# Kernel tuning notes

Measured on AMD Instinct MI355X. Metric: run time of the kernel, lower is better.

## Reference

```python
import jax, jax.numpy as jnp
import numpy as np

B, T, D, H = 4, 2048, 1024, 16
DK, DV, K, I = 48, 96, 4, 3072
EPS = 1e-5


def rmsnorm(x, w, eps=EPS):
    return x * jax.lax.rsqrt(jnp.mean(x * x, -1, keepdims=True) + eps) * w


def l2norm(x, eps=1e-6):
    return x * jax.lax.rsqrt(jnp.sum(x * x, -1, keepdims=True) + eps)


def causal_conv(x, w):
    # x: [B,T,C], w: [C,K]; causal depthwise conv (torch cross-correlation semantics)
    k = w.shape[1]
    xp = jnp.pad(x, ((0, 0), (k - 1, 0), (0, 0))).transpose(0, 2, 1)  # [B,C,T+K-1]
    y = jax.lax.conv_general_dilated(xp, w[:, None, :], (1,), 'VALID',
                                     feature_group_count=w.shape[0])
    return y.transpose(0, 2, 1)


def gated_delta_rule(q, k, v, g, beta):
    # q,k: [B,T,H,DK]  v: [B,T,H,DV]  g,beta: [B,T,H]
    scale = q.shape[-1] ** -0.5
    qT = jnp.moveaxis(q, 1, 0) * scale
    kT = jnp.moveaxis(k, 1, 0)
    vT = jnp.moveaxis(v, 1, 0)
    gT = jnp.moveaxis(g, 1, 0)
    bT = jnp.moveaxis(beta, 1, 0)
    S0 = jnp.zeros((q.shape[0], q.shape[2], q.shape[3], v.shape[3]), q.dtype)

    def step(S, inp):
        q_t, k_t, v_t, g_t, b_t = inp
        S = S * jnp.exp(g_t)[..., None, None]                      # gated decay
        v_new = (v_t - jnp.einsum('bhk,bhkv->bhv', k_t, S)) * b_t[..., None]
        S = S + k_t[..., None] * v_new[..., None, :]               # delta-rule update
        o_t = jnp.einsum('bhk,bhkv->bhv', q_t, S)
        return S, o_t

    _, o = jax.lax.scan(step, S0, (qT, kT, vT, gT, bT))
    return jnp.moveaxis(o, 0, 1)


def setup_inputs() -> dict:
    key = jax.random.key(0)
    ks = jax.random.split(key, 20)
    s = 0.02
    return {
        'hidden_states': jax.random.normal(ks[0], (B, T, D), jnp.float32),
        'norm1_w': jnp.ones((D,), jnp.float32),
        'q_w': jax.random.normal(ks[1], (D, H * DK), jnp.float32) * s,
        'k_w': jax.random.normal(ks[2], (D, H * DK), jnp.float32) * s,
        'v_w': jax.random.normal(ks[3], (D, H * DV), jnp.float32) * s,
        'conv_q_w': jax.random.normal(ks[4], (H * DK, K), jnp.float32) * 0.2,
        'conv_k_w': jax.random.normal(ks[5], (H * DK, K), jnp.float32) * 0.2,
        'conv_v_w': jax.random.normal(ks[6], (H * DV, K), jnp.float32) * 0.2,
        'b_w': jax.random.normal(ks[7], (D, H), jnp.float32) * s,
        'a_w': jax.random.normal(ks[8], (D, H), jnp.float32) * s,
        'A_log': jnp.log(jax.random.uniform(ks[9], (H,), jnp.float32, 1.0, 16.0)),
        'dt_bias': jax.random.normal(ks[10], (H,), jnp.float32) * 0.5,
        'g_w': jax.random.normal(ks[11], (D, H * DV), jnp.float32) * s,
        'o_norm_w': jnp.ones((DV,), jnp.float32),
        'o_w': jax.random.normal(ks[12], (H * DV, D), jnp.float32) * s,
        'norm2_w': jnp.ones((D,), jnp.float32),
        'gate_w': jax.random.normal(ks[13], (D, I), jnp.float32) * s,
        'up_w': jax.random.normal(ks[14], (D, I), jnp.float32) * s,
        'down_w': jax.random.normal(ks[15], (I, D), jnp.float32) * s,
    }


def reference(hidden_states, norm1_w, q_w, k_w, v_w, conv_q_w, conv_k_w, conv_v_w,
              b_w, a_w, A_log, dt_bias, g_w, o_norm_w, o_w, norm2_w,
              gate_w, up_w, down_w):
    x = hidden_states
    h = rmsnorm(x, norm1_w)
    # --- GatedDeltaNet mixer ---
    q = jax.nn.silu(causal_conv(h @ q_w, conv_q_w)).reshape(B, T, H, DK)
    k = jax.nn.silu(causal_conv(h @ k_w, conv_k_w)).reshape(B, T, H, DK)
    v = jax.nn.silu(causal_conv(h @ v_w, conv_v_w)).reshape(B, T, H, DV)
    q, k = l2norm(q), l2norm(k)
    beta = jax.nn.sigmoid(h @ b_w)                                  # [B,T,H]
    g = -jnp.exp(A_log) * jax.nn.softplus(h @ a_w + dt_bias)        # [B,T,H] mamba gate
    o = gated_delta_rule(q, k, v, g, beta)                          # [B,T,H,DV]
    gate = (h @ g_w).reshape(B, T, H, DV)
    o = rmsnorm(o, o_norm_w) * (gate * jax.nn.sigmoid(gate))        # fused gated RMSNorm
    x = x + o.reshape(B, T, H * DV) @ o_w
    # --- SwiGLU MLP ---
    h2 = rmsnorm(x, norm2_w)
    x = x + (jax.nn.silu(h2 @ gate_w) * (h2 @ up_w)) @ down_w
    return x
```

## Files before the change

kernel.cpp:

```cpp
#include <hip/hip_runtime.h>
#include <hip/hip_bf16.h>
#include <math.h>

constexpr int Bn = 4, Tn = 2048, Dn = 1024, Hn = 16, DKn = 48, DVn = 96, In = 3072;
constexpr int BT = Bn * Tn;
constexpr int HDK = Hn * DKn;
constexpr int HDV = Hn * DVn;
constexpr int QKVC = 2 * HDK + HDV;
constexpr int CC = 64;
constexpr int NC = Tn / CC;

using bf16 = __hip_bfloat16;
typedef __attribute__((ext_vector_type(8))) short bf16x8;
typedef __attribute__((ext_vector_type(4))) float f32x4;

constexpr size_t WO_HBF   = 0;
constexpr size_t WO_QKVR  = 16777216;
constexpr size_t WO_OSC   = 16777216;
constexpr size_t WO_ACT   = 16777216;
constexpr size_t WO_A     = 16777216;
constexpr size_t WO_B     = 26214400;
constexpr size_t WO_ST    = 45088768;
constexpr size_t WO_QKVC  = 67108864;
constexpr size_t WO_GATE  = 117440512;
constexpr size_t WO_X1    = 142606336;
constexpr size_t WO_BA    = 176160768;
constexpr size_t WO_GC    = 177209344;
constexpr size_t WO_T     = 177733632;
constexpr size_t WO_UV    = 194510848;
constexpr size_t WO_WB    = 219676672;
constexpr size_t WB_QKVT = 0;
constexpr size_t WB_GT   = 3145728;
constexpr size_t WB_OT   = 4718592;
constexpr size_t WB_GATET= 6291456;
constexpr size_t WB_UPT  = 9437184;
constexpr size_t WB_DOWNT= 12582912;
constexpr size_t WB_ABT  = 15728640;

__device__ __forceinline__ float sigmoidf_(float x) { return 1.f / (1.f + __expf(-x)); }
__device__ __forceinline__ float siluf(float x) { return x * sigmoidf_(x); }

__device__ __forceinline__ void glds16(const void* g, void* l) {
  __builtin_amdgcn_global_load_lds((const __attribute__((address_space(1))) void*)g,
                                   (__attribute__((address_space(3))) void*)l, 16, 0, 0);
}

__device__ __forceinline__ f32x4 mfma16(bf16x8 a, bf16x8 b, f32x4 c) {
  return __builtin_amdgcn_mfma_f32_16x16x32_bf16(a, b, c, 0, 0, 0);
}

__device__ __forceinline__ bf16x8 scale8(bf16x8 a, float s) {
  bf16x8 r;
#pragma unroll
  for (int e = 0; e < 8; e++) {
    float f = __bfloat162float(__ushort_as_bfloat16((unsigned short)a[e])) * s;
    r[e] = (short)__bfloat16_as_ushort(__float2bfloat16(f));
  }
  return r;
}

__device__ __forceinline__ float b2f(short u) {
  return __bfloat162float(__ushort_as_bfloat16((unsigned short)u));
}
__device__ __forceinline__ short f2b(float f) {
  return (short)__bfloat16_as_ushort(__float2bfloat16(f));
}

struct TcastArgs {
  const float* src[10];
  bf16* dst[10];
  int R[10], C[10], gxw[10], t0[10];
};

__global__ void tcast_all(TcastArgs a) {
  __shared__ float t[32][33];
  int bid = blockIdx.x;
  int i = 0;
#pragma unroll
  for (int k = 1; k < 10; k++) if (bid >= a.t0[k]) i = k;
  int lt = bid - a.t0[i];
  int gxw = a.gxw[i];
  int bx = lt % gxw, by = lt / gxw;
  const float* in = a.src[i];
  bf16* out = a.dst[i];
  int R = a.R[i], C = a.C[i];
  int tx = threadIdx.x, ty = threadIdx.y;
  int c0 = bx * 32, r0 = by * 32;
#pragma unroll
  for (int j = 0; j < 4; j++) {
    int r = ty + j * 8;
    float v = (c0 + tx < C) ? in[(size_t)(r0 + r) * C + c0 + tx] : 0.f;
    t[r][tx] = v;
  }
  __syncthreads();
#pragma unroll
  for (int j = 0; j < 4; j++) {
    int cc = ty + j * 8;
    if (c0 + cc < C) out[(size_t)(c0 + cc) * R + r0 + tx] = __float2bfloat16(t[tx][cc]);
  }
}

__global__ void rmsnorm_bf_k(const float* __restrict__ x, const float* __restrict__ w,
                             bf16* __restrict__ y) {
  int row = blockIdx.x;
  const float4* xr = (const float4*)(x + (size_t)row * Dn);
  int tid = threadIdx.x;
  float4 v = xr[tid];
  float ss = v.x * v.x + v.y * v.y + v.z * v.z + v.w * v.w;
  for (int m = 32; m >= 1; m >>= 1) ss += __shfl_xor(ss, m, 64);
  __shared__ float wsum[4];
  if ((tid & 63) == 0) wsum[tid >> 6] = ss;
  __syncthreads();
  ss = wsum[0] + wsum[1] + wsum[2] + wsum[3];
  float rs = rsqrtf(ss * (1.f / Dn) + 1e-5f);
  float4 wv = ((const float4*)w)[tid];
  bf16* yr = y + (size_t)row * Dn + tid * 4;
  yr[0] = __float2bfloat16(v.x * rs * wv.x);
  yr[1] = __float2bfloat16(v.y * rs * wv.y);
  yr[2] = __float2bfloat16(v.z * rs * wv.z);
  yr[3] = __float2bfloat16(v.w * rs * wv.w);
}

#define AS256(bi) (lds + (bi) * 8192)
#define BS256(bi) (lds + 32768 + (bi) * 8192)
#define STAGE256(bi, k0) do { \
    glds16(gA0 + (k0), AS256(bi) + w * 512); \
    glds16(gA1 + (k0), AS256(bi) + 4096 + w * 512); \
    glds16(gB0 + (k0), BS256(bi) + w * 512); \
    glds16(gB1 + (k0), BS256(bi) + 4096 + w * 512); \
  } while (0)

__global__ __launch_bounds__(512, 2) void gemm256(
    const bf16* __restrict__ A, const bf16* __restrict__ Bt,
    bf16* __restrict__ C0, bf16* __restrict__ C1,
    int gx, int N, int K, int mode) {
  __shared__ bf16 lds[65536];
  int nb = gx * 32;
  int q8 = nb >> 3;
  int bid = blockIdx.x;
  int sw = (bid & 7) * q8 + (bid >> 3);
  int by = sw & 31, bx = sw >> 5;
  int bm = by * 256, bn = bx * 256;
  int tid = threadIdx.x;
  int lane = tid & 63, w = tid >> 6;
  int l15 = lane & 15, lq = lane >> 4;
  int wr = w >> 2, wc = w & 3;
  int arow0 = tid >> 2;
  int srcq = (tid & 3) ^ ((arow0 >> 1) & 3);
  const bf16* gA0 = A + (size_t)(bm + arow0) * K + srcq * 8;
  const bf16* gA1 = A + (size_t)(bm + 128 + arow0) * K + srcq * 8;
  const bf16* gB0 = Bt + (size_t)(bn + arow0) * K + srcq * 8;
  const bf16* gB1 = Bt + (size_t)(bn + 128 + arow0) * K + srcq * 8;
  int slot = lq ^ ((l15 >> 1) & 3);
  f32x4 acc[8][4];
#pragma unroll
  for (int m = 0; m < 8; m++)
#pragma unroll
    for (int n = 0; n < 4; n++) acc[m][n] = (f32x4){0.f, 0.f, 0.f, 0.f};
  int NT = K >> 5;
  STAGE256(0, 0);
  STAGE256(1, 32);
  STAGE256(2, 64);
  for (int t = 0; t < NT; ++t) {
    int b = t & 3;
    if (t <= NT - 3)      { asm volatile("s_waitcnt vmcnt(8)" ::: "memory"); }
    else if (t == NT - 2) { asm volatile("s_waitcnt vmcnt(4)" ::: "memory"); }
    else                  { asm volatile("s_waitcnt vmcnt(0)" ::: "memory"); }
    __builtin_amdgcn_s_barrier();
    bf16x8 af[8], bfr[4];
#pragma unroll
    for (int m = 0; m < 8; m++)
      af[m] = *(const bf16x8*)(AS256(b) + (wr * 128 + m * 16 + l15) * 32 + slot * 8);
#pragma unroll
    for (int n = 0; n < 4; n++)
      bfr[n] = *(const bf16x8*)(BS256(b) + (wc * 64 + n * 16 + l15) * 32 + slot * 8);
    __builtin_amdgcn_s_setprio(1);
#pragma unroll
    for (int m = 0; m < 8; m++)
#pragma unroll
      for (int n = 0; n < 4; n++)
        acc[m][n] = mfma16(af[m], bfr[n], acc[m][n]);
    __builtin_amdgcn_s_setprio(0);
    if (t + 3 < NT) STAGE256((t + 3) & 3, (t + 3) * 32);
  }
  __syncthreads();
  bf16* dst; int ldc, bnl; bool doSilu;
  if (mode == 10) {
    if (bn < 3072) { dst = C0; ldc = 3072; bnl = bn; doSilu = false; }
    else           { dst = C1; ldc = 1536; bnl = bn - 3072; doSilu = false; }
  } else {
    if (bn < 3072) { dst = C0; ldc = 3072; bnl = bn; doSilu = true; }
    else           { dst = C1; ldc = 3072; bnl = bn - 3072; doSilu = false; }
  }
  bf16* cw = lds + w * 8192;
#pragma unroll
  for (int m = 0; m < 8; m++)
#pragma unroll
    for (int n = 0; n < 4; n++)
#pragma unroll
      for (int i = 0; i < 4; i++) {
        int row_l = m * 16 + lq * 4 + i;
        int col_l = n * 16 + l15;
        float v = acc[m][n][i];
        if (doSilu) v = siluf(v);
        cw[row_l * 64 + col_l] = __float2bfloat16(v);
      }
  __syncthreads();
  int r8 = lane >> 3, c8 = (lane & 7) * 8;
#pragma unroll
  for (int it = 0; it < 16; it++) {
    int row_l = it * 8 + r8;
    bf16x8 val = *(const bf16x8*)&cw[row_l * 64 + c8];
    *(bf16x8*)&dst[(size_t)(bm + wr * 128 + row_l) * ldc + bnl + wc * 64 + c8] = val;
  }
}

#define STAGE128(bi, k0) do { \
    { int c0_ = 2 * w4; \
      int arow_ = bm + c0_ * 16 + srow; \
      glds16(A + (size_t)arow_ * K + (k0) + gq * 8, &As[bi][c0_ * 512]); \
      int brow_ = bn + c0_ * 16 + srow; if (brow_ >= N) brow_ = 0; \
      glds16(Bt + (size_t)brow_ * K + (k0) + gq * 8, &Bs[bi][c0_ * 512]); \
      int c1_ = c0_ + 1; \
      int arow2_ = bm + c1_ * 16 + srow; \
      glds16(A + (size_t)arow2_ * K + (k0) + gq * 8, &As[bi][c1_ * 512]); \
      int brow2_ = bn + c1_ * 16 + srow; if (brow2_ >= N) brow2_ = 0; \
      glds16(Bt + (size_t)brow2_ * K + (k0) + gq * 8, &Bs[bi][c1_ * 512]); \
    } \
  } while (0)

__global__ __launch_bounds__(256) void gemm_mfma(
    const bf16* __restrict__ A, const bf16* __restrict__ Bt,
    void* __restrict__ Cv, const float* __restrict__ res,
    int N, int K, int ldc, int mode) {
  __shared__ bf16 As[4][4096];
  __shared__ bf16 Bs[4][4096];
  int tid = threadIdx.x, lane = tid & 63, w4 = tid >> 6;
  int bm = blockIdx.y * 128, bn = blockIdx.x * 128;
  int wr = w4 >> 1, wc = w4 & 1;
  int srow = lane >> 2;
  int gq = (lane & 3) ^ ((lane >> 3) & 3);
  int qa = (lane >> 4) ^ ((lane >> 1) & 3);
  int arow_base = wr * 64 + (lane & 15);
  int brow_base = wc * 64 + (lane & 15);
  f32x4 acc[4][4];
#pragma unroll
  for (int m = 0; m < 4; m++)
#pragma unroll
    for (int n = 0; n < 4; n++) acc[m][n] = (f32x4){0.f, 0.f, 0.f, 0.f};
  int NT = K >> 5;
  STAGE128(0, 0);
  STAGE128(1, 32);
  STAGE128(2, 64);
  for (int t = 0; t < NT; ++t) {
    int b = t & 3;
    if (t <= NT - 3)      { asm volatile("s_waitcnt vmcnt(8)" ::: "memory"); }
    else if (t == NT - 2) { asm volatile("s_waitcnt vmcnt(4)" ::: "memory"); }
    else                  { asm volatile("s_waitcnt vmcnt(0)" ::: "memory"); }
    __builtin_amdgcn_s_barrier();
    bf16x8 af[4], bfr[4];
#pragma unroll
    for (int m = 0; m < 4; m++)
      af[m] = *(const bf16x8*)&As[b][(arow_base + m * 16) * 32 + qa * 8];
#pragma unroll
    for (int n = 0; n < 4; n++)
      bfr[n] = *(const bf16x8*)&Bs[b][(brow_base + n * 16) * 32 + qa * 8];
    __builtin_amdgcn_s_setprio(1);
#pragma unroll
    for (int m = 0; m < 4; m++)
#pragma unroll
      for (int n = 0; n < 4; n++)
        acc[m][n] = mfma16(af[m], bfr[n], acc[m][n]);
    __builtin_amdgcn_s_setprio(0);
    if (t + 3 < NT) STAGE128((t + 3) & 3, (t + 3) * 32);
  }
#pragma unroll
  for (int m = 0; m < 4; m++) {
#pragma unroll
    for (int n = 0; n < 4; n++) {
      int col = bn + wc * 64 + n * 16 + (lane & 15);
      if (col >= N) continue;
#pragma unroll
      for (int i = 0; i < 4; i++) {
        int row = bm + wr * 64 + m * 16 + (lane >> 4) * 4 + i;
        float v = acc[m][n][i];
        size_t idx = (size_t)row * ldc + col;
        if (mode == 0) {
          if (res) v += res[idx];
          ((float*)Cv)[idx] = v;
        } else {
          ((bf16*)Cv)[idx] = __float2bfloat16(v);
        }
      }
    }
  }
}

__global__ __launch_bounds__(256) void convsilu2_k(const bf16* __restrict__ in,
                                                   bf16* __restrict__ outp,
                                                   const float* __restrict__ wq,
                                                   const float* __restrict__ wk,
                                                   const float* __restrict__ wv) {
  int tx = threadIdx.x & 31;
  int ty = threadIdx.x >> 5;
  int c = (blockIdx.x * 32 + tx) * 8;
  int gt = blockIdx.y * 8 + ty;
  int b = gt >> 11, t = gt & (Tn - 1);
  const float* wsrc = (c < HDK) ? (wq + c * 4)
                     : (c < 2 * HDK) ? (wk + (c - HDK) * 4)
                                     : (wv + (c - 2 * HDK) * 4);
  float4 W[8];
#pragma unroll
  for (int j = 0; j < 8; j++) W[j] = ((const float4*)wsrc)[j];
  const bf16* base = in + (size_t)b * Tn * QKVC + c;
  bf16x8 r[4];
  bf16x8 zero = {0, 0, 0, 0, 0, 0, 0, 0};
#pragma unroll
  for (int j = 0; j < 4; j++) {
    int tt = t - 3 + j;
    r[j] = (tt >= 0) ? *(const bf16x8*)(base + (size_t)tt * QKVC) : zero;
  }
  bf16x8 o;
#pragma unroll
  for (int ch = 0; ch < 8; ch++) {
    float x0 = b2f(r[0][ch]), x1 = b2f(r[1][ch]), x2 = b2f(r[2][ch]), x3 = b2f(r[3][ch]);
    float y = x0 * W[ch].x + x1 * W[ch].y + x2 * W[ch].z + x3 * W[ch].w;
    o[ch] = f2b(siluf(y));
  }
  *(bf16x8*)(outp + (size_t)gt * QKVC + c) = o;
}

__global__ __launch_bounds__(256) void l2norm_k(bf16* __restrict__ qkv) {
  int row = blockIdx.x * 256 + threadIdx.x;
  int t = row >> 5, hr = row & 31;
  bf16* p = qkv + (size_t)t * QKVC + hr * DKn;
  bf16x8 v[6];
  float ss = 0.f;
#pragma unroll
  for (int j = 0; j < 6; j++) {
    v[j] = *(const bf16x8*)(p + j * 8);
#pragma unroll
    for (int e = 0; e < 8; e++) { float f = b2f(v[j][e]); ss += f * f; }
  }
  float rs = rsqrtf(ss + 1e-6f);
#pragma unroll
  for (int j = 0; j < 6; j++) {
    bf16x8 o;
#pragma unroll
    for (int e = 0; e < 8; e++) o[e] = f2b(b2f(v[j][e]) * rs);
    *(bf16x8*)(p + j * 8) = o;
  }
}

__global__ void betag_k(float* __restrict__ ba, const float* __restrict__ A_log,
                        const float* __restrict__ dt_bias) {
  int i = blockIdx.x * blockDim.x + threadIdx.x;
  int h = i & 15, r = i >> 4;
  float bv = ba[(size_t)r * 32 + h];
  float av = ba[(size_t)r * 32 + 16 + h];
  ba[(size_t)r * 32 + h] = sigmoidf_(bv);
  float xx = av + dt_bias[h];
  float sp = (xx > 20.f) ? xx : log1pf(__expf(xx));
  ba[(size_t)r * 32 + 16 + h] = -__expf(A_log[h]) * sp;
}

__global__ __launch_bounds__(256) void dn_p1a(const bf16* __restrict__ qkv,
                                              const float* __restrict__ ba,
                                              float* __restrict__ Gc_g,
                                              bf16* __restrict__ T_g,
                                              bf16* __restrict__ Uv_g,
                                              bf16* __restrict__ A_g,
                                              bf16* __restrict__ B_g) {
  __shared__ __align__(16) char smem[62976];
  bf16 (*Kl)[72]   = (bf16(*)[72])(smem);
  bf16 (*Tl)[72]   = (bf16(*)[72])(smem + 9216);
  bf16 (*UvdT)[72] = (bf16(*)[72])(smem + 18432);
  float* Gcl = (float*)(smem + 32256);
  float* Bl  = (float*)(smem + 32512);
  bf16 (*Vl)[100]  = (bf16(*)[100])(smem + 32768);
  float (*Nl)[68]  = (float(*)[68])(smem + 45568);
  bf16 (*KTl)[72]  = (bf16(*)[72])(smem + 32768);
  bf16 (*KTbl)[72] = (bf16(*)[72])(smem + 39680);
  bf16 (*M2T)[72]  = (bf16(*)[72])(smem + 46592);
  int cid = blockIdx.x;
  int nc = cid & (NC - 1);
  int bh = cid >> 5;
  int h = bh & 15, b = bh >> 4;
  int t0 = nc * CC;
  int tid = threadIdx.x, lane = tid & 63, w = tid >> 6;
  int l15 = lane & 15, qd = lane >> 4;
  bf16 zb = __float2bfloat16(0.f);
  {
    int t = tid >> 2, p = tid & 3;
    const bf16* row = qkv + ((size_t)(b * Tn + t0 + t)) * QKVC;
    int c0 = p * 12;
#pragma unroll
    for (int j = 0; j < 12; ++j) Kl[t][c0 + j] = row[HDK + h * DKn + c0 + j];
    int j0 = p * 24;
#pragma unroll
    for (int j = 0; j < 24; ++j) Vl[t][j0 + j] = row[2 * HDK + h * DVn + j0 + j];
  }
  for (int i = tid; i < 64 * 24; i += 256) {
    int t = i / 24, c = 48 + (i % 24);
    Kl[t][c] = zb;
  }
  if (tid < 64) {
    size_t row = (size_t)(b * Tn + t0 + tid);
    float g = ba[row * 32 + 16 + h];
    float be = ba[row * 32 + h];
    float acc = g;
#pragma unroll
    for (int d = 1; d < 64; d <<= 1) {
      float o = __shfl_up(acc, d);
      if (tid >= d) acc += o;
    }
    Gcl[tid] = acc; Bl[tid] = be;
    Gc_g[(size_t)bh * Tn + t0 + tid] = acc;
  }
  __syncthreads();
  f32x4 dacc[4];
#pragma unroll
  for (int n = 0; n < 4; n++) dacc[n] = (f32x4){0.f, 0.f, 0.f, 0.f};
  {
    int arow = w * 16 + l15;
    bf16x8 a0 = *(const bf16x8*)&Kl[arow][qd * 8];
    bf16x8 a1 = *(const bf16x8*)&Kl[arow][32 + qd * 8];
#pragma unroll
    for (int n = 0; n < 4; n++) {
      int brow = n * 16 + l15;
      bf16x8 b0 = *(const bf16x8*)&Kl[brow][qd * 8];
      bf16x8 b1 = *(const bf16x8*)&Kl[brow][32 + qd * 8];
      dacc[n] = mfma16(a0, b0, dacc[n]);
      dacc[n] = mfma16(a1, b1, dacc[n]);
    }
  }
#pragma unroll
  for (int i = 0; i < 4; i++) {
    int t = w * 16 + qd * 4 + i;
    float bt = Bl[t], gt = Gcl[t];
#pragma unroll
    for (int n = 0; n < 4; n++) {
      int s = n * 16 + l15;
      Nl[t][s] = (s < t) ? bt * __expf(gt - Gcl[s]) * dacc[n][i] : 0.f;
    }
  }
  __syncthreads();
  float g63 = Gcl[63];
  int c = tid;
  if (c < 160) {
    float R[64];
    if (c < 64) {
#pragma unroll
      for (int t = 0; t < 64; ++t) R[t] = (t == c) ? 1.f : 0.f;
    } else {
      int j = c - 64;
#pragma unroll
      for (int t = 0; t < 64; ++t) R[t] = Bl[t] * __bfloat162float(Vl[t][j]);
    }
#pragma unroll
    for (int t = 1; t < 64; ++t) {
      float a0 = 0.f, a1 = 0.f, a2 = 0.f, a3 = 0.f;
#pragma unroll
      for (int s = 0; s + 3 < t; s += 4) {
        float4 n4 = *(const float4*)&Nl[t][s];
        a0 += n4.x * R[s]; a1 += n4.y * R[s + 1];
        a2 += n4.z * R[s + 2]; a3 += n4.w * R[s + 3];
      }
#pragma unroll
      for (int s = t & ~3; s < t; ++s) a0 += Nl[t][s] * R[s];
      R[t] -= ((a0 + a1) + (a2 + a3));
    }
    if (c < 64) {
#pragma unroll
      for (int t = 0; t < 64; ++t) {
        bf16 v = __float2bfloat16(R[t]);
        T_g[(size_t)cid * 4096 + t * 64 + c] = v;
        Tl[t][c] = v;
      }
    } else {
      int j = c - 64;
#pragma unroll
      for (int t = 0; t < 64; ++t) {
        Uv_g[(size_t)cid * 6144 + t * 96 + j] = __float2bfloat16(R[t]);
        UvdT[j][t] = __float2bfloat16(R[t] * __expf(g63 - Gcl[t]));
      }
    }
  }
  __syncthreads();
  for (int i = tid; i < 48 * 64; i += 256) {
    int dk = i >> 6, t = i & 63;
    bf16 kv = Kl[t][dk];
    KTl[dk][t] = kv;
    float bl = Bl[t] * __expf(Gcl[t]);
    KTbl[dk][t] = __float2bfloat16(__bfloat162float(kv) * bl);
  }
  __syncthreads();
  f32x4 m1[3];
#pragma unroll
  for (int n = 0; n < 3; n++) m1[n] = (f32x4){0.f, 0.f, 0.f, 0.f};
  {
    int arow = w * 16 + l15;
    bf16x8 a0 = *(const bf16x8*)&Tl[arow][qd * 8];
    bf16x8 a1 = *(const bf16x8*)&Tl[arow][32 + qd * 8];
#pragma unroll
    for (int n = 0; n < 3; n++) {
      int brow = n * 16 + l15;
      bf16x8 b0 = *(const bf16x8*)&KTbl[brow][qd * 8];
      bf16x8 b1 = *(const bf16x8*)&KTbl[brow][32 + qd * 8];
      m1[n] = mfma16(a0, b0, m1[n]);
      m1[n] = mfma16(a1, b1, m1[n]);
    }
  }
#pragma unroll
  for (int i = 0; i < 4; i++) {
    int tt = w * 16 + qd * 4 + i;
    float dd = __expf(g63 - Gcl[tt]);
#pragma unroll
    for (int n = 0; n < 3; n++) {
      int dk = n * 16 + l15;
      M2T[dk][tt] = __float2bfloat16(m1[n][i] * dd);
    }
  }
  __syncthreads();
  float lamC = __expf(g63);
#pragma unroll
  for (int tswap = 0; tswap < 7; tswap++) {
    int t = w + 4 * tswap;
    if (t >= 27) break;
    int mi, ni; bool isA;
    if (t < 9) { isA = true; mi = t / 3; ni = t % 3; }
    else { isA = false; mi = (t - 9) / 6; ni = (t - 9) % 6; }
    f32x4 acc = (f32x4){0.f, 0.f, 0.f, 0.f};
    int arow = mi * 16 + l15;
    bf16x8 a0 = *(const bf16x8*)&KTl[arow][qd * 8];
    bf16x8 a1 = *(const bf16x8*)&KTl[arow][32 + qd * 8];
    int brow = ni * 16 + l15;
    if (isA) {
      bf16x8 b0 = *(const bf16x8*)&M2T[brow][qd * 8];
      bf16x8 b1 = *(const bf16x8*)&M2T[brow][32 + qd * 8];
      acc = mfma16(a0, b0, acc);
      acc = mfma16(a1, b1, acc);
#pragma unroll
      for (int i = 0; i < 4; i++) {
        int row = mi * 16 + qd * 4 + i, colv = ni * 16 + l15;
        float v = ((row == colv) ? lamC : 0.f) - acc[i];
        A_g[(size_t)cid * 2304 + row * 48 + colv] = __float2bfloat16(v);
      }
    } else {
      bf16x8 b0 = *(const bf16x8*)&UvdT[brow][qd * 8];
      bf16x8 b1 = *(const bf16x8*)&UvdT[brow][32 + qd * 8];
      acc = mfma16(a0, b0, acc);
      acc = mfma16(a1, b1, acc);
#pragma unroll
      for (int i = 0; i < 4; i++) {
        int row = mi * 16 + qd * 4 + i, colv = ni * 16 + l15;
        B_g[(size_t)cid * 4608 + row * 96 + colv] = __float2bfloat16(acc[i]);
      }
    }
  }
}

__global__ __launch_bounds__(256) void dn_p2b(const bf16* __restrict__ A_g,
                                              const bf16* __restrict__ B_g,
                                              bf16* __restrict__ St_g) {
  __shared__ bf16 STl[2][96][72];
  __shared__ bf16 Al[2][48][72];
  __shared__ bf16 Bl[2][4608];
  int bh = blockIdx.x;
  int tid = threadIdx.x, lane = tid & 63, w = tid >> 6;
  int l15 = lane & 15, qd = lane >> 4;
  bf16 zb = __float2bfloat16(0.f);
  for (int i = tid; i < 2 * 96 * 72; i += 256) (&STl[0][0][0])[i] = zb;
  for (int i = tid; i < 2 * 48 * 24; i += 256) {
    int buf = i / (48 * 24), r = (i / 24) % 48, cc = 48 + (i % 24);
    Al[buf][r][cc] = zb;
  }
  bf16x8 ra0, ra1, rb0, rb1;
  unsigned int rb2;
  int e_a0 = tid * 8, e_a1 = 2048 + tid * 8;
  {
    size_t cid = (size_t)bh * NC;
    ra0 = *(const bf16x8*)(A_g + cid * 2304 + e_a0);
    if (tid < 32) ra1 = *(const bf16x8*)(A_g + cid * 2304 + e_a1);
    rb0 = *(const bf16x8*)(B_g + cid * 4608 + tid * 16);
    rb1 = *(const bf16x8*)(B_g + cid * 4608 + tid * 16 + 8);
    rb2 = *(const unsigned int*)(B_g + cid * 4608 + 4096 + tid * 2);
  }
// ... 21 lines not shown
      *(bf16x8*)(St_g + cid * 4608 + e1) = *(const bf16x8*)&STl[cur][e1 / 48][e1 % 48];
      *(unsigned int*)(St_g + cid * 4608 + e2) = *(const unsigned int*)&STl[cur][e2 / 48][e2 % 48];
    }
    float vals[5][4];
#pragma unroll
    for (int ts = 0; ts < 5; ts++) {
      int t = w + 4 * ts;
      if (t >= 18) break;
      int mi = t / 3, ni = t % 3;
      f32x4 acc = (f32x4){0.f, 0.f, 0.f, 0.f};
      int arow = mi * 16 + l15;
      bf16x8 a0 = *(const bf16x8*)&STl[cur][arow][qd * 8];
      bf16x8 a1 = *(const bf16x8*)&STl[cur][arow][32 + qd * 8];
      int brow = ni * 16 + l15;
      bf16x8 b0 = *(const bf16x8*)&Al[cur][brow][qd * 8];
      bf16x8 b1 = *(const bf16x8*)&Al[cur][brow][32 + qd * 8];
      acc = mfma16(a0, b0, acc);
      acc = mfma16(a1, b1, acc);
#pragma unroll
      for (int i = 0; i < 4; i++) {
        int dv = mi * 16 + qd * 4 + i, ii = ni * 16 + l15;
        vals[ts][i] = acc[i] + __bfloat162float(Bl[cur][ii * 96 + dv]);
      }
    }
#pragma unroll
    for (int ts = 0; ts < 5; ts++) {
      int t = w + 4 * ts;
      if (t >= 18) break;
      int mi = t / 3, ni = t % 3;
#pragma unroll
      for (int i = 0; i < 4; i++) {
        int dv = mi * 16 + qd * 4 + i, ii = ni * 16 + l15;
        STl[nxt][dv][ii] = __float2bfloat16(vals[ts][i]);
      }
    }
    if (c + 1 <= NC - 2) {
      *(bf16x8*)&Al[nxt][e_a0 / 48][e_a0 % 48] = ra0;
      if (tid < 32) *(bf16x8*)&Al[nxt][e_a1 / 48][e_a1 % 48] = ra1;
      *(bf16x8*)&Bl[nxt][tid * 16] = rb0;
      *(bf16x8*)&Bl[nxt][tid * 16 + 8] = rb1;
      *(unsigned int*)&Bl[nxt][4096 + tid * 2] = rb2;
      if (c + 2 <= NC - 2) {
        size_t cid2 = (size_t)bh * NC + c + 2;
        ra0 = *(const bf16x8*)(A_g + cid2 * 2304 + e_a0);
        if (tid < 32) ra1 = *(const bf16x8*)(A_g + cid2 * 2304 + e_a1);
        rb0 = *(const bf16x8*)(B_g + cid2 * 4608 + tid * 16);
        rb1 = *(const bf16x8*)(B_g + cid2 * 4608 + tid * 16 + 8);
        rb2 = *(const unsigned int*)(B_g + cid2 * 4608 + 4096 + tid * 2);
      }
    }
    __syncthreads();
  }
  {
    size_t cid = (size_t)bh * NC + (NC - 1);
    int cur = (NC - 1) & 1;
    int e0 = tid * 8, e1 = 2048 + tid * 8, e2 = 4096 + tid * 2;
    *(bf16x8*)(St_g + cid * 4608 + e0) = *(const bf16x8*)&STl[cur][e0 / 48][e0 % 48];
    *(bf16x8*)(St_g + cid * 4608 + e1) = *(const bf16x8*)&STl[cur][e1 / 48][e1 % 48];
    *(unsigned int*)(St_g + cid * 4608 + e2) = *(const unsigned int*)&STl[cur][e2 / 48][e2 % 48];
  }
}

__global__ __launch_bounds__(256) void dn_p2c(const bf16* __restrict__ qkv,
                                              const float* __restrict__ ba,
                                              const float* __restrict__ Gc_g,
                                              const bf16* __restrict__ T_g,
                                              const bf16* __restrict__ Uv_g,
                                              const bf16* __restrict__ St_g,
                                              const bf16* __restrict__ gate,
                                              const float* __restrict__ onw,
                                              bf16* __restrict__ attn) {
  __shared__ bf16 Kl[64][72], Ql[64][72], Tl[64][72], Ml[64][72];
  __shared__ bf16 G1T[96][72], UT[96][72], STb[96][72];
  __shared__ float Gcl[64], Bl[64];
  __shared__ float onwl[96];
  int cid = blockIdx.x;
  int nc = cid & (NC - 1);
  int bh = cid >> 5;
  int h = bh & 15, b = bh >> 4;
  int t0 = nc * CC;
  int tid = threadIdx.x, lane = tid & 63, w = tid >> 6;
  int l15 = lane & 15, qd = lane >> 4;
  const float scale = 0.14433756729740643f;
  bf16 zb = __float2bfloat16(0.f);
  {
    int t = tid >> 2, p = tid & 3;
    size_t grow = (size_t)(b * Tn + t0 + t);
    const bf16* row = qkv + grow * QKVC;
    int c0 = p * 12;
#pragma unroll
    for (int j = 0; j < 12; ++j) {
      int cc = c0 + j;
      Kl[t][cc] = row[HDK + h * DKn + cc];
      Ql[t][cc] = __float2bfloat16(__bfloat162float(row[h * DKn + cc]) * scale);
    }
    if (p == 0) { Gcl[t] = Gc_g[(size_t)bh * Tn + t0 + t]; Bl[t] = ba[grow * 32 + h]; }
  }
  if (tid < 96) onwl[tid] = onw[tid];
  for (int i = tid; i < 64 * 16; i += 256) {
    int t = i >> 4, cc = 48 + (i & 15);
    Kl[t][cc] = zb; Ql[t][cc] = zb;
  }
  for (int i = tid; i < 4096; i += 256)
    (&Tl[0][0])[(i >> 6) * 72 + (i & 63)] = T_g[(size_t)cid * 4096 + i];
  for (int i = tid; i < 4608; i += 256)
    STb[i / 48][i % 48] = St_g[(size_t)cid * 4608 + i];
  for (int i = tid; i < 96 * 16; i += 256)
    STb[i >> 4][48 + (i & 15)] = zb;
  __syncthreads();
  f32x4 acc[6];
#pragma unroll
  for (int n = 0; n < 6; n++) acc[n] = (f32x4){0.f, 0.f, 0.f, 0.f};
  {
    int arow = w * 16 + l15;
    bf16x8 a0 = *(const bf16x8*)&Kl[arow][qd * 8];
    bf16x8 a1 = *(const bf16x8*)&Kl[arow][32 + qd * 8];
#pragma unroll
    for (int n = 0; n < 6; n++) {
      int brow = n * 16 + l15;
      bf16x8 b0 = *(const bf16x8*)&STb[brow][qd * 8];
      bf16x8 b1 = *(const bf16x8*)&STb[brow][32 + qd * 8];
      acc[n] = mfma16(a0, b0, acc[n]);
      acc[n] = mfma16(a1, b1, acc[n]);
    }
  }
#pragma unroll
  for (int i = 0; i < 4; i++) {
    int tt = w * 16 + qd * 4 + i;
    float sc = Bl[tt] * __expf(Gcl[tt]);
#pragma unroll
    for (int n = 0; n < 6; n++)
      G1T[n * 16 + l15][tt] = __float2bfloat16(acc[n][i] * sc);
  }
  __syncthreads();
#pragma unroll
  for (int n = 0; n < 6; n++) acc[n] = (f32x4){0.f, 0.f, 0.f, 0.f};
  {
    int arow = w * 16 + l15;
    bf16x8 a0 = *(const bf16x8*)&Tl[arow][qd * 8];
    bf16x8 a1 = *(const bf16x8*)&Tl[arow][32 + qd * 8];
#pragma unroll
    for (int n = 0; n < 6; n++) {
      int brow = n * 16 + l15;
      bf16x8 b0 = *(const bf16x8*)&G1T[brow][qd * 8];
      bf16x8 b1 = *(const bf16x8*)&G1T[brow][32 + qd * 8];
      acc[n] = mfma16(a0, b0, acc[n]);
      acc[n] = mfma16(a1, b1, acc[n]);
    }
  }
#pragma unroll
  for (int i = 0; i < 4; i++) {
    int tt = w * 16 + qd * 4 + i;
#pragma unroll
    for (int n = 0; n < 6; n++) {
      int dv = n * 16 + l15;
      float uv = __bfloat162float(Uv_g[(size_t)cid * 6144 + tt * 96 + dv]);
      UT[dv][tt] = __float2bfloat16(uv - acc[n][i]);
    }
  }
  f32x4 qk[4];
#pragma unroll
  for (int n = 0; n < 4; n++) qk[n] = (f32x4){0.f, 0.f, 0.f, 0.f};
  {
    int arow = w * 16 + l15;
    bf16x8 a0 = *(const bf16x8*)&Ql[arow][qd * 8];
    bf16x8 a1 = *(const bf16x8*)&Ql[arow][32 + qd * 8];
#pragma unroll
    for (int n = 0; n < 4; n++) {
      int brow = n * 16 + l15;
      bf16x8 b0 = *(const bf16x8*)&Kl[brow][qd * 8];
      bf16x8 b1 = *(const bf16x8*)&Kl[brow][32 + qd * 8];
      qk[n] = mfma16(a0, b0, qk[n]);
      qk[n] = mfma16(a1, b1, qk[n]);
    }
  }
#pragma unroll
  for (int i = 0; i < 4; i++) {
    int tt = w * 16 + qd * 4 + i;
    float gt = Gcl[tt];
#pragma unroll
    for (int n = 0; n < 4; n++) {
      int ss = n * 16 + l15;
      float m = (ss <= tt) ? qk[n][i] * __expf(gt - Gcl[ss]) : 0.f;
      Ml[tt][ss] = __float2bfloat16(m);
    }
  }
  __syncthreads();
#pragma unroll
  for (int n = 0; n < 6; n++) acc[n] = (f32x4){0.f, 0.f, 0.f, 0.f};
  {
    int arow = w * 16 + l15;
    float lam = __expf(Gcl[arow]);
    bf16x8 a0 = scale8(*(const bf16x8*)&Ql[arow][qd * 8], lam);
    bf16x8 a1 = scale8(*(const bf16x8*)&Ql[arow][32 + qd * 8], lam);
    bf16x8 m0 = *(const bf16x8*)&Ml[arow][qd * 8];
    bf16x8 m1 = *(const bf16x8*)&Ml[arow][32 + qd * 8];
#pragma unroll
    for (int n = 0; n < 6; n++) {
      int brow = n * 16 + l15;
      bf16x8 b0 = *(const bf16x8*)&STb[brow][qd * 8];
      bf16x8 b1 = *(const bf16x8*)&STb[brow][32 + qd * 8];
      acc[n] = mfma16(a0, b0, acc[n]);
      acc[n] = mfma16(a1, b1, acc[n]);
      bf16x8 u0 = *(const bf16x8*)&UT[brow][qd * 8];
      bf16x8 u1 = *(const bf16x8*)&UT[brow][32 + qd * 8];
      acc[n] = mfma16(m0, u0, acc[n]);
      acc[n] = mfma16(m1, u1, acc[n]);
    }
  }
#pragma unroll
  for (int i = 0; i < 4; i++) {
    int tt = w * 16 + qd * 4 + i;
    float ss = 0.f;
#pragma unroll
    for (int n = 0; n < 6; n++) ss += acc[n][i] * acc[n][i];
    ss += __shfl_xor(ss, 1, 64);
    ss += __shfl_xor(ss, 2, 64);
    ss += __shfl_xor(ss, 4, 64);
    ss += __shfl_xor(ss, 8, 64);
    float rs = rsqrtf(ss * (1.f / DVn) + 1e-5f);
    size_t orow = ((size_t)(b * Tn + t0 + tt)) * HDV + h * DVn;
#pragma unroll
    for (int n = 0; n < 6; n++) {
      int dv = n * 16 + l15;
      float g = __bfloat162float(gate[orow + dv]);
      attn[orow + dv] = __float2bfloat16(acc[n][i] * rs * onwl[dv] * siluf(g));
    }
  }
}

__global__ __launch_bounds__(256) void silumul_bf_k(bf16* __restrict__ a,
                                                    const bf16* __restrict__ b) {
  size_t i = ((size_t)blockIdx.x * 256 + threadIdx.x) * 8;
  bf16x8 av = *(const bf16x8*)(a + i);
  bf16x8 bv = *(const bf16x8*)(b + i);
  bf16x8 r;
#pragma unroll
  for (int e = 0; e < 8; e++) r[e] = f2b(b2f(av[e]) * b2f(bv[e]));
  *(bf16x8*)(a + i) = r;
}

extern "C" void kernel_launch(void* const* d_in, const int* in_sizes, int n_in,
                              void* d_out, int out_size, void* d_ws, size_t ws_size,
                              hipStream_t stream) {
  const float* x       = (const float*)d_in[0];
  const float* norm1_w = (const float*)d_in[1];
  const float* q_w     = (const float*)d_in[2];
  const float* k_w     = (const float*)d_in[3];
  const float* v_w     = (const float*)d_in[4];
  const float* cq_w    = (const float*)d_in[5];
  const float* ck_w    = (const float*)d_in[6];
  const float* cv_w    = (const float*)d_in[7];
  const float* b_w     = (const float*)d_in[8];
  const float* a_w     = (const float*)d_in[9];
  const float* A_log   = (const float*)d_in[10];
  const float* dt_bias = (const float*)d_in[11];
  const float* g_w     = (const float*)d_in[12];
  const float* o_norm_w= (const float*)d_in[13];
  const float* o_w     = (const float*)d_in[14];
  const float* norm2_w = (const float*)d_in[15];
  const float* gate_w  = (const float*)d_in[16];
  const float* up_w    = (const float*)d_in[17];
  const float* down_w  = (const float*)d_in[18];
  char* wsb = (char*)d_ws;
  float* out = (float*)d_out;

  bf16*  hbf   = (bf16*)(wsb + WO_HBF);
  bf16*  qkvr  = (bf16*)(wsb + WO_QKVR);
  bf16*  qkvc  = (bf16*)(wsb + WO_QKVC);
  bf16*  upb   = (bf16*)(wsb + WO_QKVC);
  bf16*  attn  = (bf16*)(wsb + WO_OSC);
  bf16*  actb  = (bf16*)(wsb + WO_ACT);
  bf16*  gateb = (bf16*)(wsb + WO_GATE);
  float* x1    = (float*)(wsb + WO_X1);
  float* ba    = (float*)(wsb + WO_BA);
  float* Gc    = (float*)(wsb + WO_GC);
  bf16*  Tg    = (bf16*)(wsb + WO_T);
  bf16*  Uvg   = (bf16*)(wsb + WO_UV);
  bf16*  A_g   = (bf16*)(wsb + WO_A);
  bf16*  B_g   = (bf16*)(wsb + WO_B);
  bf16*  St_g  = (bf16*)(wsb + WO_ST);
  bf16*  wb    = (bf16*)(wsb + WO_WB);

  {
    TcastArgs ta;
    const float* srcs[10] = {q_w, k_w, v_w, g_w, o_w, gate_w, up_w, down_w, b_w, a_w};
    bf16* dsts[10] = {wb + WB_QKVT, wb + WB_QKVT + 768 * 1024, wb + WB_QKVT + 1536 * 1024,
                      wb + WB_GT, wb + WB_OT, wb + WB_GATET, wb + WB_UPT, wb + WB_DOWNT,
                      wb + WB_ABT, wb + WB_ABT + 16 * 1024};
    int Rs[10] = {1024, 1024, 1024, 1024, 1536, 1024, 1024, 3072, 1024, 1024};
    int Cs[10] = {768, 768, 1536, 1536, 1024, 3072, 3072, 1024, 16, 16};
    int off = 0;
    for (int i = 0; i < 10; i++) {
      ta.src[i] = srcs[i]; ta.dst[i] = dsts[i];
      ta.R[i] = Rs[i]; ta.C[i] = Cs[i];
      ta.gxw[i] = (Cs[i] + 31) / 32;
      ta.t0[i] = off;
      off += ta.gxw[i] * (Rs[i] / 32);
    }
    tcast_all<<<off, dim3(32, 8), 0, stream>>>(ta);
  }

  rmsnorm_bf_k<<<BT, 256, 0, stream>>>(x, norm1_w, hbf);
  gemm256<<<576, 512, 0, stream>>>(hbf, wb + WB_QKVT, qkvr, gateb, 18, 4608, 1024, 10);
  gemm_mfma<<<dim3(1, 64), 256, 0, stream>>>(hbf, wb + WB_ABT, ba, nullptr, 32, 1024, 32, 0);
  convsilu2_k<<<dim3(QKVC / 256, BT / 8), 256, 0, stream>>>(qkvr, qkvc, cq_w, ck_w, cv_w);
  l2norm_k<<<(BT * 32) / 256, 256, 0, stream>>>(qkvc);
  betag_k<<<(BT * Hn) / 256, 256, 0, stream>>>(ba, A_log, dt_bias);
  dn_p1a<<<Bn * Hn * NC, 256, 0, stream>>>(qkvc, ba, Gc, Tg, Uvg, A_g, B_g);
  dn_p2b<<<Bn * Hn, 256, 0, stream>>>(A_g, B_g, St_g);
  dn_p2c<<<Bn * Hn * NC, 256, 0, stream>>>(qkvc, ba, Gc, Tg, Uvg, St_g, gateb, o_norm_w, attn);
  gemm_mfma<<<dim3(8, 64), 256, 0, stream>>>(attn, wb + WB_OT, x1, x, 1024, 1536, 1024, 0);
  rmsnorm_bf_k<<<BT, 256, 0, stream>>>(x1, norm2_w, hbf);
  gemm256<<<768, 512, 0, stream>>>(hbf, wb + WB_GATET, actb, upb, 24, 6144, 1024, 11);
  silumul_bf_k<<<(BT * In) / (8 * 256), 256, 0, stream>>>(actb, upb);
  gemm_mfma<<<dim3(8, 64), 256, 0, stream>>>(actb, wb + WB_DOWNT, out, x1, 1024, 3072, 1024, 0);
}
```

Baseline: 715.0 us.

## Double-buffer LDS fragment loads in register to overlap with MFMA in GEMMs

Both GEMM kernels now keep two sets of register fragments and load the next k-step's A/B fragments from LDS before issuing the current step's MFMAs. The loop is manually unrolled by two, with waitcnt and barrier placement adjusted. The aim is to hide LDS read latency behind matrix-core work. The cost is more VGPRs, which could lower occupancy in the 256-tile kernel that has launch_bounds(512,2), and the 4-deep LDS ring now relies on tighter vmcnt and barrier bookkeeping.

```diff
diff --git a/kernel.cpp b/kernel.cpp
--- a/kernel.cpp
+++ b/kernel.cpp
@@ -128,6 +128,23 @@
     glds16(gA1 + (k0), AS256(bi) + 4096 + w * 512); \
     glds16(gB0 + (k0), BS256(bi) + w * 512); \
     glds16(gB1 + (k0), BS256(bi) + 4096 + w * 512); \
+  } while (0)
+#define LOADFRAG256(dstA, dstB, bi) do { \
+    _Pragma("unroll") \
+    for (int m_ = 0; m_ < 8; m_++) \
+      dstA[m_] = *(const bf16x8*)(AS256(bi) + (wr * 128 + m_ * 16 + l15) * 32 + slot * 8); \
+    _Pragma("unroll") \
+    for (int n_ = 0; n_ < 4; n_++) \
+      dstB[n_] = *(const bf16x8*)(BS256(bi) + (wc * 64 + n_ * 16 + l15) * 32 + slot * 8); \
+  } while (0)
+#define MFMA256(srcA, srcB) do { \
+    __builtin_amdgcn_s_setprio(1); \
+    _Pragma("unroll") \
+    for (int m_ = 0; m_ < 8; m_++) \
+      _Pragma("unroll") \
+      for (int n_ = 0; n_ < 4; n_++) \
+        acc[m_][n_] = mfma16(srcA[m_], srcB[n_], acc[m_][n_]); \
+    __builtin_amdgcn_s_setprio(0); \
   } while (0)
 
 __global__ __launch_bounds__(512, 2) void gemm256(
@@ -161,27 +178,25 @@
   STAGE256(0, 0);
   STAGE256(1, 32);
   STAGE256(2, 64);
-  for (int t = 0; t < NT; ++t) {
-    int b = t & 3;
-    if (t <= NT - 3)      { asm volatile("s_waitcnt vmcnt(8)" ::: "memory"); }
-    else if (t == NT - 2) { asm volatile("s_waitcnt vmcnt(4)" ::: "memory"); }
-    else                  { asm volatile("s_waitcnt vmcnt(0)" ::: "memory"); }
+  bf16x8 afA[8], bfA[4], afB[8], bfB[4];
+  asm volatile("s_waitcnt vmcnt(8)" ::: "memory");
+  __builtin_amdgcn_s_barrier();
+  LOADFRAG256(afA, bfA, 0);
+  for (int t = 0; t < NT; t += 2) {
+    if (t + 2 < NT) { asm volatile("s_waitcnt vmcnt(4)" ::: "memory"); }
+    else            { asm volatile("s_waitcnt vmcnt(0)" ::: "memory"); }
     __builtin_amdgcn_s_barrier();
-    bf16x8 af[8], bfr[4];
-#pragma unroll
-    for (int m = 0; m < 8; m++)
-      af[m] = *(const bf16x8*)(AS256(b) + (wr * 128 + m * 16 + l15) * 32 + slot * 8);
-#pragma unroll
-    for (int n = 0; n < 4; n++)
-      bfr[n] = *(const bf16x8*)(BS256(b) + (wc * 64 + n * 16 + l15) * 32 + slot * 8);
-    __builtin_amdgcn_s_setprio(1);
-#pragma unroll
-    for (int m = 0; m < 8; m++)
-#pragma unroll
-      for (int n = 0; n < 4; n++)
-        acc[m][n] = mfma16(af[m], bfr[n], acc[m][n]);
-    __builtin_amdgcn_s_setprio(0);
+    if (t + 1 < NT) { int b1 = (t + 1) & 3; LOADFRAG256(afB, bfB, b1); }
+    MFMA256(afA, bfA);
     if (t + 3 < NT) STAGE256((t + 3) & 3, (t + 3) * 32);
+    if (t + 1 < NT) {
+      if (t + 3 < NT) { asm volatile("s_waitcnt vmcnt(4)" ::: "memory"); }
+      else            { asm volatile("s_waitcnt vmcnt(0)" ::: "memory"); }
+      __builtin_amdgcn_s_barrier();
+      if (t + 2 < NT) { int b2 = (t + 2) & 3; LOADFRAG256(afA, bfA, b2); }
+      MFMA256(afB, bfB);
+      if (t + 4 < NT) STAGE256((t + 4) & 3, (t + 4) * 32);
+    }
   }
   __syncthreads();
   bf16* dst; int ldc, bnl; bool doSilu;
@@ -227,6 +242,23 @@
       int brow2_ = bn + c1_ * 16 + srow; if (brow2_ >= N) brow2_ = 0; \
       glds16(Bt + (size_t)brow2_ * K + (k0) + gq * 8, &Bs[bi][c1_ * 512]); \
     } \
+  } while (0)
+#define LOADFRAG128(dstA, dstB, bi) do { \
+    _Pragma("unroll") \
+    for (int m_ = 0; m_ < 4; m_++) \
+      dstA[m_] = *(const bf16x8*)&As[bi][(arow_base + m_ * 16) * 32 + qa * 8]; \
+    _Pragma("unroll") \
+    for (int n_ = 0; n_ < 4; n_++) \
+      dstB[n_] = *(const bf16x8*)&Bs[bi][(brow_base + n_ * 16) * 32 + qa * 8]; \
+  } while (0)
+#define MFMA128(srcA, srcB) do { \
+    __builtin_amdgcn_s_setprio(1); \
+    _Pragma("unroll") \
+    for (int m_ = 0; m_ < 4; m_++) \
+      _Pragma("unroll") \
+      for (int n_ = 0; n_ < 4; n_++) \
+        acc[m_][n_] = mfma16(srcA[m_], srcB[n_], acc[m_][n_]); \
+    __builtin_amdgcn_s_setprio(0); \
   } while (0)
 
 __global__ __launch_bounds__(256) void gemm_mfma(
@@ -252,27 +284,25 @@
   STAGE128(0, 0);
   STAGE128(1, 32);
   STAGE128(2, 64);
-  for (int t = 0; t < NT; ++t) {
-    int b = t & 3;
-    if (t <= NT - 3)      { asm volatile("s_waitcnt vmcnt(8)" ::: "memory"); }
-    else if (t == NT - 2) { asm volatile("s_waitcnt vmcnt(4)" ::: "memory"); }
-    else                  { asm volatile("s_waitcnt vmcnt(0)" ::: "memory"); }
+  bf16x8 afA[4], bfA[4], afB[4], bfB[4];
+  asm volatile("s_waitcnt vmcnt(8)" ::: "memory");
+  __builtin_amdgcn_s_barrier();
+  LOADFRAG128(afA, bfA, 0);
+  for (int t = 0; t < NT; t += 2) {
+    if (t + 2 < NT) { asm volatile("s_waitcnt vmcnt(4)" ::: "memory"); }
+    else            { asm volatile("s_waitcnt vmcnt(0)" ::: "memory"); }
     __builtin_amdgcn_s_barrier();
-    bf16x8 af[4], bfr[4];
-#pragma unroll
-    for (int m = 0; m < 4; m++)
-      af[m] = *(const bf16x8*)&As[b][(arow_base + m * 16) * 32 + qa * 8];
-#pragma unroll
-    for (int n = 0; n < 4; n++)
-      bfr[n] = *(const bf16x8*)&Bs[b][(brow_base + n * 16) * 32 + qa * 8];
-    __builtin_amdgcn_s_setprio(1);
-#pragma unroll
-    for (int m = 0; m < 4; m++)
-#pragma unroll
-      for (int n = 0; n < 4; n++)
-        acc[m][n] = mfma16(af[m], bfr[n], acc[m][n]);
-    __builtin_amdgcn_s_setprio(0);
+    if (t + 1 < NT) { int b1 = (t + 1) & 3; LOADFRAG128(afB, bfB, b1); }
+    MFMA128(afA, bfA);
     if (t + 3 < NT) STAGE128((t + 3) & 3, (t + 3) * 32);
+    if (t + 1 < NT) {
+      if (t + 3 < NT) { asm volatile("s_waitcnt vmcnt(4)" ::: "memory"); }
+      else            { asm volatile("s_waitcnt vmcnt(0)" ::: "memory"); }
+      __builtin_amdgcn_s_barrier();
+      if (t + 2 < NT) { int b2 = (t + 2) & 3; LOADFRAG128(afA, bfA, b2); }
+      MFMA128(afB, bfB);
+      if (t + 4 < NT) STAGE128((t + 4) & 3, (t + 4) * 32);
+    }
   }
 #pragma unroll
   for (int m = 0; m < 4; m++) {
```

New measurement: 722.6 us. About the same (+1.1%).

## Run GEMM kernels with 1024-thread blocks and smaller per-wave tiles

Applied to the files above, without the earlier changes.

Both GEMM kernels switch to 16 waves per block. Each wave computes a smaller sub-tile (64x64 in gemm256, 32x32 in gemm_mfma) and issues fewer global-to-LDS loads per stage, with the vmcnt waits rescaled to match. The gemm256 epilogue also gains an XOR swizzle on the LDS staging buffer to avoid bank conflicts. The intent is more waves for latency hiding with fewer registers per wave, at the cost of less MFMA work per LDS fragment read and more barrier overhead per block.

```diff
diff --git a/kernel.cpp b/kernel.cpp
--- a/kernel.cpp
+++ b/kernel.cpp
@@ -125,12 +125,10 @@
 #define BS256(bi) (lds + 32768 + (bi) * 8192)
 #define STAGE256(bi, k0) do { \
     glds16(gA0 + (k0), AS256(bi) + w * 512); \
-    glds16(gA1 + (k0), AS256(bi) + 4096 + w * 512); \
     glds16(gB0 + (k0), BS256(bi) + w * 512); \
-    glds16(gB1 + (k0), BS256(bi) + 4096 + w * 512); \
   } while (0)
 
-__global__ __launch_bounds__(512, 2) void gemm256(
+__global__ __launch_bounds__(1024) void gemm256(
     const bf16* __restrict__ A, const bf16* __restrict__ Bt,
     bf16* __restrict__ C0, bf16* __restrict__ C1,
     int gx, int N, int K, int mode) {
@@ -148,13 +146,11 @@
   int arow0 = tid >> 2;
   int srcq = (tid & 3) ^ ((arow0 >> 1) & 3);
   const bf16* gA0 = A + (size_t)(bm + arow0) * K + srcq * 8;
-  const bf16* gA1 = A + (size_t)(bm + 128 + arow0) * K + srcq * 8;
   const bf16* gB0 = Bt + (size_t)(bn + arow0) * K + srcq * 8;
-  const bf16* gB1 = Bt + (size_t)(bn + 128 + arow0) * K + srcq * 8;
   int slot = lq ^ ((l15 >> 1) & 3);
-  f32x4 acc[8][4];
-#pragma unroll
-  for (int m = 0; m < 8; m++)
+  f32x4 acc[4][4];
+#pragma unroll
+  for (int m = 0; m < 4; m++)
 #pragma unroll
     for (int n = 0; n < 4; n++) acc[m][n] = (f32x4){0.f, 0.f, 0.f, 0.f};
   int NT = K >> 5;
@@ -163,20 +159,20 @@
   STAGE256(2, 64);
   for (int t = 0; t < NT; ++t) {
     int b = t & 3;
-    if (t <= NT - 3)      { asm volatile("s_waitcnt vmcnt(8)" ::: "memory"); }
-    else if (t == NT - 2) { asm volatile("s_waitcnt vmcnt(4)" ::: "memory"); }
+    if (t <= NT - 3)      { asm volatile("s_waitcnt vmcnt(4)" ::: "memory"); }
+    else if (t == NT - 2) { asm volatile("s_waitcnt vmcnt(2)" ::: "memory"); }
     else                  { asm volatile("s_waitcnt vmcnt(0)" ::: "memory"); }
     __builtin_amdgcn_s_barrier();
-    bf16x8 af[8], bfr[4];
-#pragma unroll
-    for (int m = 0; m < 8; m++)
-      af[m] = *(const bf16x8*)(AS256(b) + (wr * 128 + m * 16 + l15) * 32 + slot * 8);
+    bf16x8 af[4], bfr[4];
+#pragma unroll
+    for (int m = 0; m < 4; m++)
+      af[m] = *(const bf16x8*)(AS256(b) + (wr * 64 + m * 16 + l15) * 32 + slot * 8);
 #pragma unroll
     for (int n = 0; n < 4; n++)
       bfr[n] = *(const bf16x8*)(BS256(b) + (wc * 64 + n * 16 + l15) * 32 + slot * 8);
     __builtin_amdgcn_s_setprio(1);
 #pragma unroll
-    for (int m = 0; m < 8; m++)
+    for (int m = 0; m < 4; m++)
 #pragma unroll
       for (int n = 0; n < 4; n++)
         acc[m][n] = mfma16(af[m], bfr[n], acc[m][n]);
@@ -192,9 +188,9 @@
     if (bn < 3072) { dst = C0; ldc = 3072; bnl = bn; doSilu = true; }
     else           { dst = C1; ldc = 3072; bnl = bn - 3072; doSilu = false; }
   }
-  bf16* cw = lds + w * 8192;
-#pragma unroll
-  for (int m = 0; m < 8; m++)
+  bf16* cw = lds + w * 4096;
+#pragma unroll
+  for (int m = 0; m < 4; m++)
 #pragma unroll
     for (int n = 0; n < 4; n++)
 #pragma unroll
@@ -203,86 +199,83 @@
         int col_l = n * 16 + l15;
         float v = acc[m][n][i];
         if (doSilu) v = siluf(v);
-        cw[row_l * 64 + col_l] = __float2bfloat16(v);
+        cw[row_l * 64 + (col_l ^ ((row_l & 7) << 3))] = __float2bfloat16(v);
       }
   __syncthreads();
-  int r8 = lane >> 3, c8 = (lane & 7) * 8;
-#pragma unroll
-  for (int it = 0; it < 16; it++) {
+  int r8 = lane >> 3, cblk = lane & 7;
+#pragma unroll
+  for (int it = 0; it < 8; it++) {
     int row_l = it * 8 + r8;
-    bf16x8 val = *(const bf16x8*)&cw[row_l * 64 + c8];
-    *(bf16x8*)&dst[(size_t)(bm + wr * 128 + row_l) * ldc + bnl + wc * 64 + c8] = val;
-  }
-}
-
-#define STAGE128(bi, k0) do { \
-    { int c0_ = 2 * w4; \
-      int arow_ = bm + c0_ * 16 + srow; \
-      glds16(A + (size_t)arow_ * K + (k0) + gq * 8, &As[bi][c0_ * 512]); \
-      int brow_ = bn + c0_ * 16 + srow; if (brow_ >= N) brow_ = 0; \
-      glds16(Bt + (size_t)brow_ * K + (k0) + gq * 8, &Bs[bi][c0_ * 512]); \
-      int c1_ = c0_ + 1; \
-      int arow2_ = bm + c1_ * 16 + srow; \
-      glds16(A + (size_t)arow2_ * K + (k0) + gq * 8, &As[bi][c1_ * 512]); \
-      int brow2_ = bn + c1_ * 16 + srow; if (brow2_ >= N) brow2_ = 0; \
-      glds16(Bt + (size_t)brow2_ * K + (k0) + gq * 8, &Bs[bi][c1_ * 512]); \
-    } \
-  } while (0)
-
-__global__ __launch_bounds__(256) void gemm_mfma(
+    int sblk = cblk ^ (row_l & 7);
+    bf16x8 val = *(const bf16x8*)&cw[row_l * 64 + sblk * 8];
+    *(bf16x8*)&dst[(size_t)(bm + wr * 64 + row_l) * ldc + bnl + wc * 64 + cblk * 8] = val;
+  }
+}
+
+__global__ __launch_bounds__(1024) void gemm_mfma(
     const bf16* __restrict__ A, const bf16* __restrict__ Bt,
     void* __restrict__ Cv, const float* __restrict__ res,
     int N, int K, int ldc, int mode) {
   __shared__ bf16 As[4][4096];
   __shared__ bf16 Bs[4][4096];
-  int tid = threadIdx.x, lane = tid & 63, w4 = tid >> 6;
+  int tid = threadIdx.x, lane = tid & 63, w = tid >> 6;
   int bm = blockIdx.y * 128, bn = blockIdx.x * 128;
-  int wr = w4 >> 1, wc = w4 & 1;
-  int srow = lane >> 2;
-  int gq = (lane & 3) ^ ((lane >> 3) & 3);
-  int qa = (lane >> 4) ^ ((lane >> 1) & 3);
-  int arow_base = wr * 64 + (lane & 15);
-  int brow_base = wc * 64 + (lane & 15);
-  f32x4 acc[4][4];
-#pragma unroll
-  for (int m = 0; m < 4; m++)
-#pragma unroll
-    for (int n = 0; n < 4; n++) acc[m][n] = (f32x4){0.f, 0.f, 0.f, 0.f};
+  int l15 = lane & 15, lq = lane >> 4;
+  int wr = w >> 2, wc = w & 3;
+  int r0 = (tid & 511) >> 2;
+  int sq = (tid & 3) ^ ((r0 >> 1) & 3);
+  const bf16* g0;
+  bf16* lb;
+  if (w < 8) {
+    g0 = A + (size_t)(bm + r0) * K + sq * 8;
+    lb = &As[0][w * 512];
+  } else {
+    int br = bn + r0; if (br >= N) br = 0;
+    g0 = Bt + (size_t)br * K + sq * 8;
+    lb = &Bs[0][(w - 8) * 512];
+  }
+#define STAGE128X(bi, k0) glds16(g0 + (k0), lb + (bi) * 4096)
+  int slot = lq ^ ((l15 >> 1) & 3);
+  f32x4 acc[2][2];
+#pragma unroll
+  for (int m = 0; m < 2; m++)
+#pragma unroll
+    for (int n = 0; n < 2; n++) acc[m][n] = (f32x4){0.f, 0.f, 0.f, 0.f};
   int NT = K >> 5;
-  STAGE128(0, 0);
-  STAGE128(1, 32);
-  STAGE128(2, 64);
+  STAGE128X(0, 0);
+  STAGE128X(1, 32);
+  STAGE128X(2, 64);
   for (int t = 0; t < NT; ++t) {
     int b = t & 3;
-    if (t <= NT - 3)      { asm volatile("s_waitcnt vmcnt(8)" ::: "memory"); }
-    else if (t == NT - 2) { asm volatile("s_waitcnt vmcnt(4)" ::: "memory"); }
+    if (t <= NT - 3)      { asm volatile("s_waitcnt vmcnt(2)" ::: "memory"); }
+    else if (t == NT - 2) { asm volatile("s_waitcnt vmcnt(1)" ::: "memory"); }
     else                  { asm volatile("s_waitcnt vmcnt(0)" ::: "memory"); }
     __builtin_amdgcn_s_barrier();
-    bf16x8 af[4], bfr[4];
-#pragma unroll
-    for (int m = 0; m < 4; m++)
-      af[m] = *(const bf16x8*)&As[b][(arow_base + m * 16) * 32 + qa * 8];
-#pragma unroll
-    for (int n = 0; n < 4; n++)
-      bfr[n] = *(const bf16x8*)&Bs[b][(brow_base + n * 16) * 32 + qa * 8];
+    bf16x8 af[2], bfr[2];
+#pragma unroll
+    for (int m = 0; m < 2; m++)
+      af[m] = *(const bf16x8*)&As[b][(wr * 32 + m * 16 + l15) * 32 + slot * 8];
+#pragma unroll
+    for (int n = 0; n < 2; n++)
+      bfr[n] = *(const bf16x8*)&Bs[b][(wc * 32 + n * 16 + l15) * 32 + slot * 8];
     __builtin_amdgcn_s_setprio(1);
 #pragma unroll
-    for (int m = 0; m < 4; m++)
-#pragma unroll
-      for (int n = 0; n < 4; n++)
+    for (int m = 0; m < 2; m++)
+#pragma unroll
+      for (int n = 0; n < 2; n++)
         acc[m][n] = mfma16(af[m], bfr[n], acc[m][n]);
     __builtin_amdgcn_s_setprio(0);
-    if (t + 3 < NT) STAGE128((t + 3) & 3, (t + 3) * 32);
-  }
-#pragma unroll
-  for (int m = 0; m < 4; m++) {
-#pragma unroll
-    for (int n = 0; n < 4; n++) {
-      int col = bn + wc * 64 + n * 16 + (lane & 15);
+    if (t + 3 < NT) STAGE128X((t + 3) & 3, (t + 3) * 32);
+  }
+#pragma unroll
+  for (int m = 0; m < 2; m++) {
+#pragma unroll
+    for (int n = 0; n < 2; n++) {
+      int col = bn + wc * 32 + n * 16 + l15;
       if (col >= N) continue;
 #pragma unroll
       for (int i = 0; i < 4; i++) {
-        int row = bm + wr * 64 + m * 16 + (lane >> 4) * 4 + i;
+        int row = bm + wr * 32 + m * 16 + lq * 4 + i;
         float v = acc[m][n][i];
         size_t idx = (size_t)row * ldc + col;
         if (mode == 0) {
@@ -910,17 +903,17 @@
   }
 
   rmsnorm_bf_k<<<BT, 256, 0, stream>>>(x, norm1_w, hbf);
-  gemm256<<<576, 512, 0, stream>>>(hbf, wb + WB_QKVT, qkvr, gateb, 18, 4608, 1024, 10);
-  gemm_mfma<<<dim3(1, 64), 256, 0, stream>>>(hbf, wb + WB_ABT, ba, nullptr, 32, 1024, 32, 0);
+  gemm256<<<576, 1024, 0, stream>>>(hbf, wb + WB_QKVT, qkvr, gateb, 18, 4608, 1024, 10);
+  gemm_mfma<<<dim3(1, 64), 1024, 0, stream>>>(hbf, wb + WB_ABT, ba, nullptr, 32, 1024, 32, 0);
   convsilu2_k<<<dim3(QKVC / 256, BT / 8), 256, 0, stream>>>(qkvr, qkvc, cq_w, ck_w, cv_w);
   l2norm_k<<<(BT * 32) / 256, 256, 0, stream>>>(qkvc);
   betag_k<<<(BT * Hn) / 256, 256, 0, stream>>>(ba, A_log, dt_bias);
   dn_p1a<<<Bn * Hn * NC, 256, 0, stream>>>(qkvc, ba, Gc, Tg, Uvg, A_g, B_g);
   dn_p2b<<<Bn * Hn, 256, 0, stream>>>(A_g, B_g, St_g);
   dn_p2c<<<Bn * Hn * NC, 256, 0, stream>>>(qkvc, ba, Gc, Tg, Uvg, St_g, gateb, o_norm_w, attn);
-  gemm_mfma<<<dim3(8, 64), 256, 0, stream>>>(attn, wb + WB_OT, x1, x, 1024, 1536, 1024, 0);
+  gemm_mfma<<<dim3(8, 64), 1024, 0, stream>>>(attn, wb + WB_OT, x1, x, 1024, 1536, 1024, 0);
   rmsnorm_bf_k<<<BT, 256, 0, stream>>>(x1, norm2_w, hbf);
-  gemm256<<<768, 512, 0, stream>>>(hbf, wb + WB_GATET, actb, upb, 24, 6144, 1024, 11);
+  gemm256<<<768, 1024, 0, stream>>>(hbf, wb + WB_GATET, actb, upb, 24, 6144, 1024, 11);
   silumul_bf_k<<<(BT * In) / (8 * 256), 256, 0, stream>>>(actb, upb);
-  gemm_mfma<<<dim3(8, 64), 256, 0, stream>>>(actb, wb + WB_DOWNT, out, x1, 1024, 3072, 1024, 0);
-}
+  gemm_mfma<<<dim3(8, 64), 1024, 0, stream>>>(actb, wb + WB_DOWNT, out, x1, 1024, 3072, 1024, 0);
+}
```

Measured after the change: 665.3 us. 7.0% less time.
